# Performance work log

Measured on AMD Instinct MI355X. Metric: run time of the kernel, lower is better.

The kernel has to match this reference:

```python
import jax, jax.numpy as jnp
import numpy as np

K = 7          # neighbor volumes
PS = 7         # patch size (unfold.ps)
C = 3          # image channels -> F = C*PS*PS = 147
H = 256
W = 256
PAD = PS // 2
HP, WP = H + 2 * PAD, W + 2 * PAD


def _unfold(img, qindex):
    # img: [Ch, H, W]; extract PS x PS patches centered at each query pixel.
    # returns [Ch, Q, PS, PS]
    padded = jnp.pad(img, ((0, 0), (PAD, PAD), (PAD, PAD)))
    i = qindex // W
    j = qindex % W
    d = jnp.arange(PS)
    rows = i[:, None, None] + d[None, :, None]   # [Q,PS,1] in padded coords
    cols = j[:, None, None] + d[None, None, :]   # [Q,1,PS]
    return padded[:, rows, cols]                 # [Ch,Q,PS,PS]


def _fold(patches, qindex):
    # patches: [Q, Ch, PS, PS]; scatter-add centered patches into image canvas.
    Ch = patches.shape[1]
    i = qindex // W
    j = qindex % W
    d = jnp.arange(PS)
    rows = i[:, None, None] + d[None, :, None]
    cols = j[:, None, None] + d[None, None, :]
    flat = (rows * WP + cols).reshape(-1)                         # [Q*PS*PS]
    vals = patches.transpose(0, 2, 3, 1).reshape(-1, Ch)          # [Q*PS*PS, Ch]
    canvas = jnp.zeros((HP * WP, Ch), patches.dtype).at[flat].add(vals)
    canvas = canvas.reshape(HP, WP, Ch).transpose(2, 0, 1)
    return canvas[:, PAD:PAD + H, PAD:PAD + W]                    # [Ch,H,W]


def _nnn(D, log_temp, k):
    # Neural nearest neighbors (N3Net): D [Q,O] = -squared dists, log_temp [Q,1]
    logits = D / jnp.exp(log_temp)
    ws = []
    for _ in range(k):
        w = jax.nn.softmax(logits, axis=-1)
        ws.append(w)
        logits = logits + jnp.log(jnp.clip(1.0 - w, 1e-6))
    return jnp.stack(ws, axis=-1)  # [Q,O,k]


def setup_inputs() -> dict:
    key = jax.random.key(0)
    k1, k2, k3, k4, k5 = jax.random.split(key, 5)
    Q = H * W
    N = Q
    O = 32
    E = 64
    F = C * PS * PS
    return {
        "x": jax.random.normal(k1, (N, F), jnp.float32),
        "xe": jax.random.normal(k2, (N, E), jnp.float32),
        "ye": jax.random.normal(k3, (Q, E), jnp.float32),
        "log_temp": jax.random.normal(k4, (1, 1, H, W), jnp.float32),
        "cand_inds": jax.random.randint(k5, (Q, O), 0, N, jnp.int32),
        "qindex": jnp.arange(Q, dtype=jnp.int32),
    }


def reference(x, xe, ye, log_temp, cand_inds, qindex):
    Q, O = cand_inds.shape
    # --- search: L2^2 distances to O candidate database items per query ---
    xg = xe[cand_inds]                                            # [Q,O,E]
    d2 = (jnp.sum(ye * ye, -1, keepdims=True)
          + jnp.sum(xg * xg, -1)
          - 2.0 * jnp.einsum('qe,qoe->qo', ye, xg))               # [Q,O]
    dists = -d2
    # --- per-query log temperature: unfold + avgpool over the patch ---
    lt = _unfold(log_temp[0], qindex)                             # [1,Q,PS,PS]
    lt = lt.reshape(Q, PS * PS, 1).mean(axis=1)                   # [Q,1] (avgpool)
    # --- neural nearest neighbors weights ---
    Wmat = _nnn(dists, lt, K)                                     # [Q,O,K]
    # --- wpsum: weighted patch sum for each of the K neighbor volumes ---
    xp = x[cand_inds]                                             # [Q,O,F]
    z = jnp.einsum('qof,qok->kqf', xp, Wmat)                      # [K,Q,F]
    # rearrange 'k q (c ph pw) -> q (k c) ph pw'
    z = z.reshape(K, Q, C, PS, PS).transpose(1, 0, 2, 3, 4).reshape(Q, K * C, PS, PS)
    # --- fold aggregated patches and the weight counts back to image ---
    vid = _fold(z, qindex)                                        # [K*C,H,W]
    wvid = _fold(jnp.ones_like(z), qindex)                        # [K*C,H,W]
    return vid, wvid
```

## Files before the change

kernel.cpp:

```cpp
#include <hip/hip_runtime.h>
#include <hip/hip_bf16.h>
#include <math.h>

namespace {
constexpr int KNB  = 7;
constexpr int PS   = 7;
constexpr int CCH  = 3;
constexpr int IH   = 256;
constexpr int IW   = 256;
constexpr int PADR = 3;
constexpr int QN   = IH * IW;
constexpr int ON   = 32;
constexpr int EN   = 64;
constexpr int FN   = CCH * PS * PS;
constexpr int KC   = KNB * CCH;
constexpr int TQY  = 8;
constexpr int TQX  = 4;
constexpr int CHY  = TQY + PS - 1;
constexpr int CHX  = TQX + PS - 1;
constexpr int CELEM = KC * CHY * CHX;
constexpr int NW   = 4;
constexpr int NBX  = IW / TQX;
constexpr int NBY  = IH / TQY;
}

__device__ __forceinline__ float bf16_to_f(unsigned short u) {
    union { unsigned int i; float f; } c;
    c.i = ((unsigned int)u) << 16;
    return c.f;
}

__global__ __launch_bounds__(256) void conv_kernel(
    const float* __restrict__ x, unsigned short* __restrict__ xb, int n4)
{
    int i = blockIdx.x * blockDim.x + threadIdx.x;
    if (i >= n4) return;
    float4 v = ((const float4*)x)[i];
    ushort4 o;
    o.x = __hip_bfloat16_raw(__float2bfloat16(v.x)).x;
    o.y = __hip_bfloat16_raw(__float2bfloat16(v.y)).x;
    o.z = __hip_bfloat16_raw(__float2bfloat16(v.z)).x;
    o.w = __hip_bfloat16_raw(__float2bfloat16(v.w)).x;
    ((ushort4*)xb)[i] = o;
}

template <bool BF16, typename XT>
__global__ __launch_bounds__(256, 4) void n3_tile_kernel(
    const XT*    __restrict__ x,
    const float* __restrict__ xe,
    const float* __restrict__ ye,
    const float* __restrict__ log_temp,
    const int*   __restrict__ cand,
    const int*   __restrict__ qindex,
    float*       __restrict__ vid)
{
    __shared__ float canvas[CELEM];
    __shared__ float w_lds[NW][ON][8];
    __shared__ int   off_lds[NW][ON];

    const int wib  = threadIdx.x >> 6;
    const int lane = threadIdx.x & 63;
    const int by   = blockIdx.x / NBX;
    const int bx   = blockIdx.x - by * NBX;
    const int y0   = by * TQY;
    const int x0   = bx * TQX;

    for (int i = threadIdx.x; i < CELEM; i += 256) canvas[i] = 0.f;
    __syncthreads();

    for (int ty = 0; ty < TQY; ++ty) {
        const int q = (y0 + ty) * IW + (x0 + wib);

        const int qpix = qindex[q];
        const int qi = qpix / IW;
        const int qj = qpix - qi * IW;

        float ltv = 0.f;
        if (lane < PS * PS) {
            int pi = lane / PS, pj = lane % PS;
            int yy = qi + pi - PADR, xx = qj + pj - PADR;
            if (yy >= 0 && yy < IH && xx >= 0 && xx < IW)
                ltv = log_temp[yy * IW + xx];
        }
        #pragma unroll
        for (int s = 32; s >= 1; s >>= 1) ltv += __shfl_xor(ltv, s);
        const float itemp = expf(-ltv * (1.f / 49.f));

        const int o = lane & 31;
        const int h = lane >> 5;
        const int cidx = cand[q * ON + o];
        if (lane < ON) off_lds[wib][o] = cidx * FN;
        {
            const float4* xr = (const float4*)(xe + (size_t)cidx * EN) + h * 8;
            const float4* yr = (const float4*)(ye + (size_t)q * EN) + h * 8;
            float dot = 0.f, xn = 0.f, yn = 0.f;
            #pragma unroll
            for (int e = 0; e < 8; ++e) {
                float4 a = xr[e];
                float4 b = yr[e];
                dot += a.x * b.x + a.y * b.y + a.z * b.z + a.w * b.w;
                xn  += a.x * a.x + a.y * a.y + a.z * a.z + a.w * a.w;
                yn  += b.x * b.x + b.y * b.y + b.z * b.z + b.w * b.w;
            }
            float part = xn + yn - 2.f * dot;
            part += __shfl_xor(part, 32);
            float logit = -part * itemp;
            float wk[KNB];
            #pragma unroll
            for (int k = 0; k < KNB; ++k) {
                float m = logit;
                #pragma unroll
                for (int s = 16; s >= 1; s >>= 1) m = fmaxf(m, __shfl_xor(m, s));
                float ev = expf(logit - m);
                float ssum = ev;
                #pragma unroll
                for (int s = 16; s >= 1; s >>= 1) ssum += __shfl_xor(ssum, s);
                float w = ev / ssum;
                wk[k] = w;
                logit += logf(fmaxf(1.f - w, 1e-6f));
            }
            if (lane < ON) {
                #pragma unroll
                for (int k = 0; k < KNB; ++k) w_lds[wib][lane][k] = wk[k];
            }
        }

        #pragma unroll
        for (int it = 0; it < 3; ++it) {
            const int f = it * 64 + lane;
            const bool act = f < FN;
            float acc[KNB];
            #pragma unroll
            for (int k = 0; k < KNB; ++k) acc[k] = 0.f;
            #pragma unroll 8
            for (int oo = 0; oo < ON; ++oo) {
                const int off = off_lds[wib][oo];
                float xv;
                if (BF16) xv = act ? bf16_to_f((unsigned short)x[off + f]) : 0.f;
                else      xv = act ? (float)x[off + f] : 0.f;
                #pragma unroll
                for (int k = 0; k < KNB; ++k) acc[k] += xv * w_lds[wib][oo][k];
            }
            if (act) {
                const int c  = f / (PS * PS);
                const int r  = f - c * (PS * PS);
                const int pi = r / PS;
                const int pj = r - pi * PS;
                const int ly = qi + pi - y0;
                const int lx = qj + pj - x0;
                #pragma unroll
                for (int k = 0; k < KNB; ++k)
                    atomicAdd(&canvas[(k * CCH + c) * (CHY * CHX) + ly * CHX + lx], acc[k]);
            }
        }
    }

    __syncthreads();

    for (int i = threadIdx.x; i < CELEM; i += 256) {
        const float v = canvas[i];
        if (v != 0.f) {
            const int ch  = i / (CHY * CHX);
            const int rem = i - ch * (CHY * CHX);
            const int ly  = rem / CHX;
            const int lx  = rem - ly * CHX;
            const int gy  = y0 - PADR + ly;
            const int gx  = x0 - PADR + lx;
            if (gy >= 0 && gy < IH && gx >= 0 && gx < IW)
                atomicAdd(&vid[(size_t)ch * QN + gy * IW + gx], v);
        }
    }
}

__global__ __launch_bounds__(256) void wvid_kernel(float* __restrict__ wvid) {
    int idx = blockIdx.x * blockDim.x + threadIdx.x;
    if (idx >= QN) return;
    int y  = idx / IW;
    int xx = idx - y * IW;
    int cy = min(PS - 1, y  + PADR) - max(0, y  - (IH - 1 - PADR)) + 1;
    int cx = min(PS - 1, xx + PADR) - max(0, xx - (IW - 1 - PADR)) + 1;
    float v = (float)(cy * cx);
    #pragma unroll
    for (int ch = 0; ch < KC; ++ch) wvid[(size_t)ch * QN + idx] = v;
}

extern "C" void kernel_launch(void* const* d_in, const int* in_sizes, int n_in,
                              void* d_out, int out_size, void* d_ws, size_t ws_size,
                              hipStream_t stream) {
    const float* x    = (const float*)d_in[0];
    const float* xe   = (const float*)d_in[1];
    const float* ye   = (const float*)d_in[2];
    const float* ltm  = (const float*)d_in[3];
    const int*   cand = (const int*)d_in[4];
    const int*   qidx = (const int*)d_in[5];

    float* vid  = (float*)d_out;
    float* wvid = vid + (size_t)KC * QN;

    hipMemsetAsync(vid, 0, (size_t)KC * QN * sizeof(float), stream);

    const size_t xelems = (size_t)QN * FN;
    const size_t xbytes = xelems * sizeof(unsigned short);

    if (ws_size >= xbytes) {
        unsigned short* xb = (unsigned short*)d_ws;
        const int n4 = (int)(xelems / 4);
        conv_kernel<<<(n4 + 255) / 256, 256, 0, stream>>>(x, xb, n4);
        n3_tile_kernel<true, unsigned short><<<NBX * NBY, 256, 0, stream>>>(
            xb, xe, ye, ltm, cand, qidx, vid);
    } else {
        n3_tile_kernel<false, float><<<NBX * NBY, 256, 0, stream>>>(
            x, xe, ye, ltm, cand, qidx, vid);
    }
    wvid_kernel<<<(QN + 255) / 256, 256, 0, stream>>>(wvid);
}
```

Measured before the change: 672.5 us.

## Stage gathered bf16 patch rows into LDS with double-buffered async loads

Pads the bf16 copy of x to 192 elements per row so each gathered candidate row can be fetched with 16-byte global_load_lds transfers. Each wave double-buffers groups of 8 candidate rows in LDS and overlaps the loads with the weighted accumulation. The loads for the first group are issued before the distance and softmax work. This replaces scattered 2-byte global gathers with wide asynchronous copies, and all three feature chunks are accumulated together from LDS. In exchange the LDS footprint grows, occupancy drops to 3 blocks per CU, and correctness depends on hand-placed vmcnt waits.

```diff
diff --git a/kernel.cpp b/kernel.cpp
--- a/kernel.cpp
+++ b/kernel.cpp
@@ -22,6 +22,10 @@
 constexpr int NW   = 4;
 constexpr int NBX  = IW / TQX;
 constexpr int NBY  = IH / TQY;
+constexpr int RP   = 192;
+constexpr int RPB  = RP * 2;
+constexpr int QROWS = 8;
+constexpr int QELEM = QROWS * RP;
 }
 
 __device__ __forceinline__ float bf16_to_f(unsigned short u) {
@@ -30,23 +34,33 @@
     return c.f;
 }
 
-__global__ __launch_bounds__(256) void conv_kernel(
-    const float* __restrict__ x, unsigned short* __restrict__ xb, int n4)
+__device__ __forceinline__ void gload_lds16(const void* g, void* l) {
+    __builtin_amdgcn_global_load_lds(
+        (const __attribute__((address_space(1))) unsigned int*)g,
+        (__attribute__((address_space(3))) unsigned int*)l, 16, 0, 0);
+}
+
+__global__ __launch_bounds__(256) void conv192_kernel(
+    const float* __restrict__ x, unsigned short* __restrict__ xb)
 {
-    int i = blockIdx.x * blockDim.x + threadIdx.x;
-    if (i >= n4) return;
-    float4 v = ((const float4*)x)[i];
-    ushort4 o;
-    o.x = __hip_bfloat16_raw(__float2bfloat16(v.x)).x;
-    o.y = __hip_bfloat16_raw(__float2bfloat16(v.y)).x;
-    o.z = __hip_bfloat16_raw(__float2bfloat16(v.z)).x;
-    o.w = __hip_bfloat16_raw(__float2bfloat16(v.w)).x;
-    ((ushort4*)xb)[i] = o;
-}
-
-template <bool BF16, typename XT>
-__global__ __launch_bounds__(256, 4) void n3_tile_kernel(
-    const XT*    __restrict__ x,
+    int t = blockIdx.x * blockDim.x + threadIdx.x;
+    const int total = QN * (RP / 8);
+    if (t >= total) return;
+    int row = t / (RP / 8);
+    int c8  = (t - row * (RP / 8)) * 8;
+    const float* src = x + (size_t)row * FN;
+    union { unsigned short u[8]; uint4 q; } v;
+    #pragma unroll
+    for (int j = 0; j < 8; ++j) {
+        int e = c8 + j;
+        float f = (e < FN) ? src[e] : 0.f;
+        v.u[j] = __hip_bfloat16_raw(__float2bfloat16(f)).x;
+    }
+    *(uint4*)((char*)xb + (size_t)row * RPB + c8 * 2) = v.q;
+}
+
+__global__ __launch_bounds__(256, 3) void n3_staged_kernel(
+    const unsigned short* __restrict__ xb,
     const float* __restrict__ xe,
     const float* __restrict__ ye,
     const float* __restrict__ log_temp,
@@ -57,6 +71,7 @@
     __shared__ float canvas[CELEM];
     __shared__ float w_lds[NW][ON][8];
     __shared__ int   off_lds[NW][ON];
+    __shared__ unsigned short xstage[NW][2][QELEM];
 
     const int wib  = threadIdx.x >> 6;
     const int lane = threadIdx.x & 63;
@@ -70,10 +85,25 @@
 
     for (int ty = 0; ty < TQY; ++ty) {
         const int q = (y0 + ty) * IW + (x0 + wib);
-
         const int qpix = qindex[q];
         const int qi = qpix / IW;
         const int qj = qpix - qi * IW;
+
+        const int o = lane & 31;
+        const int cidx = cand[q * ON + o];
+        if (lane < ON) off_lds[wib][o] = cidx * RPB;
+
+        {
+            const int* offr = &off_lds[wib][0];
+            #pragma unroll
+            for (int i = 0; i < 3; ++i) {
+                int slot = i * 64 + lane;
+                int r = slot / 24;
+                int c = slot - r * 24;
+                gload_lds16((const char*)xb + offr[r] + c * 16,
+                            (char*)&xstage[wib][0][0] + i * 1024);
+            }
+        }
 
         float ltv = 0.f;
         if (lane < PS * PS) {
@@ -86,11 +116,8 @@
         for (int s = 32; s >= 1; s >>= 1) ltv += __shfl_xor(ltv, s);
         const float itemp = expf(-ltv * (1.f / 49.f));
 
-        const int o = lane & 31;
-        const int h = lane >> 5;
-        const int cidx = cand[q * ON + o];
-        if (lane < ON) off_lds[wib][o] = cidx * FN;
         {
+            const int h = lane >> 5;
             const float4* xr = (const float4*)(xe + (size_t)cidx * EN) + h * 8;
             const float4* yr = (const float4*)(ye + (size_t)q * EN) + h * 8;
             float dot = 0.f, xn = 0.f, yn = 0.f;
@@ -125,23 +152,55 @@
             }
         }
 
+        float acc[3][KNB];
+        #pragma unroll
+        for (int it = 0; it < 3; ++it)
+            #pragma unroll
+            for (int k = 0; k < KNB; ++k) acc[it][k] = 0.f;
+
+        #pragma unroll
+        for (int qt = 0; qt < 4; ++qt) {
+            const int par = qt & 1;
+            if (qt < 3) {
+                const int* offr = &off_lds[wib][(qt + 1) * QROWS];
+                #pragma unroll
+                for (int i = 0; i < 3; ++i) {
+                    int slot = i * 64 + lane;
+                    int r = slot / 24;
+                    int c = slot - r * 24;
+                    gload_lds16((const char*)xb + offr[r] + c * 16,
+                                (char*)&xstage[wib][par ^ 1][0] + i * 1024);
+                }
+                asm volatile("s_waitcnt vmcnt(3)" ::: "memory");
+            } else {
+                asm volatile("s_waitcnt vmcnt(0)" ::: "memory");
+            }
+            __builtin_amdgcn_sched_barrier(0);
+
+            const unsigned short* xs = &xstage[wib][par][0];
+            #pragma unroll
+            for (int r = 0; r < QROWS; ++r) {
+                const int oo = qt * QROWS + r;
+                const float4 wa = *(const float4*)&w_lds[wib][oo][0];
+                const float4 wb = *(const float4*)&w_lds[wib][oo][4];
+                #pragma unroll
+                for (int it = 0; it < 3; ++it) {
+                    const float xv = bf16_to_f(xs[r * RP + it * 64 + lane]);
+                    acc[it][0] += xv * wa.x;
+                    acc[it][1] += xv * wa.y;
+                    acc[it][2] += xv * wa.z;
+                    acc[it][3] += xv * wa.w;
+                    acc[it][4] += xv * wb.x;
+                    acc[it][5] += xv * wb.y;
+                    acc[it][6] += xv * wb.z;
+                }
+            }
+        }
+
         #pragma unroll
         for (int it = 0; it < 3; ++it) {
             const int f = it * 64 + lane;
-            const bool act = f < FN;
-            float acc[KNB];
-            #pragma unroll
-            for (int k = 0; k < KNB; ++k) acc[k] = 0.f;
-            #pragma unroll 8
-            for (int oo = 0; oo < ON; ++oo) {
-                const int off = off_lds[wib][oo];
-                float xv;
-                if (BF16) xv = act ? bf16_to_f((unsigned short)x[off + f]) : 0.f;
-                else      xv = act ? (float)x[off + f] : 0.f;
-                #pragma unroll
-                for (int k = 0; k < KNB; ++k) acc[k] += xv * w_lds[wib][oo][k];
-            }
-            if (act) {
+            if (f < FN) {
                 const int c  = f / (PS * PS);
                 const int r  = f - c * (PS * PS);
                 const int pi = r / PS;
@@ -150,7 +209,8 @@
                 const int lx = qj + pj - x0;
                 #pragma unroll
                 for (int k = 0; k < KNB; ++k)
-                    atomicAdd(&canvas[(k * CCH + c) * (CHY * CHX) + ly * CHX + lx], acc[k]);
+                    atomicAdd(&canvas[(k * CCH + c) * (CHY * CHX) + ly * CHX + lx],
+                              acc[it][k]);
             }
         }
     }
@@ -172,6 +232,130 @@
     }
 }
 
+__global__ __launch_bounds__(256, 4) void n3_fallback_kernel(
+    const float* __restrict__ x,
+    const float* __restrict__ xe,
+    const float* __restrict__ ye,
+    const float* __restrict__ log_temp,
+    const int*   __restrict__ cand,
+    const int*   __restrict__ qindex,
+    float*       __restrict__ vid)
+{
+    __shared__ float canvas[CELEM];
+    __shared__ float w_lds[NW][ON][8];
+    __shared__ int   off_lds[NW][ON];
+
+    const int wib  = threadIdx.x >> 6;
+    const int lane = threadIdx.x & 63;
+    const int by   = blockIdx.x / NBX;
+    const int bx   = blockIdx.x - by * NBX;
+    const int y0   = by * TQY;
+    const int x0   = bx * TQX;
+
+    for (int i = threadIdx.x; i < CELEM; i += 256) canvas[i] = 0.f;
+    __syncthreads();
+
+    for (int ty = 0; ty < TQY; ++ty) {
+        const int q = (y0 + ty) * IW + (x0 + wib);
+        const int qpix = qindex[q];
+        const int qi = qpix / IW;
+        const int qj = qpix - qi * IW;
+
+        float ltv = 0.f;
+        if (lane < PS * PS) {
+            int pi = lane / PS, pj = lane % PS;
+            int yy = qi + pi - PADR, xx = qj + pj - PADR;
+            if (yy >= 0 && yy < IH && xx >= 0 && xx < IW)
+                ltv = log_temp[yy * IW + xx];
+        }
+        #pragma unroll
+        for (int s = 32; s >= 1; s >>= 1) ltv += __shfl_xor(ltv, s);
+        const float itemp = expf(-ltv * (1.f / 49.f));
+
+        const int o = lane & 31;
+        const int h = lane >> 5;
+        const int cidx = cand[q * ON + o];
+        if (lane < ON) off_lds[wib][o] = cidx * FN;
+        {
+            const float4* xr = (const float4*)(xe + (size_t)cidx * EN) + h * 8;
+            const float4* yr = (const float4*)(ye + (size_t)q * EN) + h * 8;
+            float dot = 0.f, xn = 0.f, yn = 0.f;
+            #pragma unroll
+            for (int e = 0; e < 8; ++e) {
+                float4 a = xr[e];
+                float4 b = yr[e];
+                dot += a.x * b.x + a.y * b.y + a.z * b.z + a.w * b.w;
+                xn  += a.x * a.x + a.y * a.y + a.z * a.z + a.w * a.w;
+                yn  += b.x * b.x + b.y * b.y + b.z * b.z + b.w * b.w;
+            }
+            float part = xn + yn - 2.f * dot;
+            part += __shfl_xor(part, 32);
+            float logit = -part * itemp;
+            float wk[KNB];
+            #pragma unroll
+            for (int k = 0; k < KNB; ++k) {
+                float m = logit;
+                #pragma unroll
+                for (int s = 16; s >= 1; s >>= 1) m = fmaxf(m, __shfl_xor(m, s));
+                float ev = expf(logit - m);
+                float ssum = ev;
+                #pragma unroll
+                for (int s = 16; s >= 1; s >>= 1) ssum += __shfl_xor(ssum, s);
+                float w = ev / ssum;
+                wk[k] = w;
+                logit += logf(fmaxf(1.f - w, 1e-6f));
+            }
+            if (lane < ON) {
+                #pragma unroll
+                for (int k = 0; k < KNB; ++k) w_lds[wib][lane][k] = wk[k];
+            }
+        }
+
+        #pragma unroll
+        for (int it = 0; it < 3; ++it) {
+            const int f = it * 64 + lane;
+            const bool act = f < FN;
+            float acc[KNB];
+            #pragma unroll
+            for (int k = 0; k < KNB; ++k) acc[k] = 0.f;
+            #pragma unroll 8
+            for (int oo = 0; oo < ON; ++oo) {
+                const int off = off_lds[wib][oo];
+                const float xv = act ? x[off + f] : 0.f;
+                #pragma unroll
+                for (int k = 0; k < KNB; ++k) acc[k] += xv * w_lds[wib][oo][k];
+            }
+            if (act) {
+                const int c  = f / (PS * PS);
+                const int r  = f - c * (PS * PS);
+                const int pi = r / PS;
+                const int pj = r - pi * PS;
+                const int ly = qi + pi - y0;
+                const int lx = qj + pj - x0;
+                #pragma unroll
+                for (int k = 0; k < KNB; ++k)
+                    atomicAdd(&canvas[(k * CCH + c) * (CHY * CHX) + ly * CHX + lx], acc[k]);
+            }
+        }
+    }
+
+    __syncthreads();
+
+    for (int i = threadIdx.x; i < CELEM; i += 256) {
+        const float v = canvas[i];
+        if (v != 0.f) {
+            const int ch  = i / (CHY * CHX);
+            const int rem = i - ch * (CHY * CHX);
+            const int ly  = rem / CHX;
+            const int lx  = rem - ly * CHX;
+            const int gy  = y0 - PADR + ly;
+            const int gx  = x0 - PADR + lx;
+            if (gy >= 0 && gy < IH && gx >= 0 && gx < IW)
+                atomicAdd(&vid[(size_t)ch * QN + gy * IW + gx], v);
+        }
+    }
+}
+
 __global__ __launch_bounds__(256) void wvid_kernel(float* __restrict__ wvid) {
     int idx = blockIdx.x * blockDim.x + threadIdx.x;
     if (idx >= QN) return;
@@ -199,17 +383,16 @@
 
     hipMemsetAsync(vid, 0, (size_t)KC * QN * sizeof(float), stream);
 
-    const size_t xelems = (size_t)QN * FN;
-    const size_t xbytes = xelems * sizeof(unsigned short);
+    const size_t xbytes = (size_t)QN * RPB;
 
     if (ws_size >= xbytes) {
         unsigned short* xb = (unsigned short*)d_ws;
-        const int n4 = (int)(xelems / 4);
-        conv_kernel<<<(n4 + 255) / 256, 256, 0, stream>>>(x, xb, n4);
-        n3_tile_kernel<true, unsigned short><<<NBX * NBY, 256, 0, stream>>>(
+        const int nconv = QN * (RP / 8);
+        conv192_kernel<<<(nconv + 255) / 256, 256, 0, stream>>>(x, xb);
+        n3_staged_kernel<<<NBX * NBY, 256, 0, stream>>>(
             xb, xe, ye, ltm, cand, qidx, vid);
     } else {
-        n3_tile_kernel<false, float><<<NBX * NBY, 256, 0, stream>>>(
+        n3_fallback_kernel<<<NBX * NBY, 256, 0, stream>>>(
             x, xe, ye, ltm, cand, qidx, vid);
     }
     wvid_kernel<<<(QN + 255) / 256, 256, 0, stream>>>(wvid);
```

New measurement: 1.039 ms. 1.55x slower.
